# Kernel optimization log

Hardware: AMD Instinct MI355X
Metric: run time of the kernel (lower is better)

The kernel has to match this reference:

```python
import jax, jax.numpy as jnp
import numpy as np

N_NODES = 50000
N_EDGES = 800000
D_IN = 128
D_OUT = 128


def _seg_mean(values, seg_ids, num_segments):
    # values: [E, D] gathered messages; seg_ids: [E] destination ids
    s = jax.ops.segment_sum(values, seg_ids, num_segments=num_segments)
    deg = jax.ops.segment_sum(jnp.ones((values.shape[0],), values.dtype), seg_ids,
                              num_segments=num_segments)
    # DGL mean aggregation yields 0 for zero in-degree nodes
    return jnp.where(deg[:, None] > 0, s / jnp.maximum(deg, 1.0)[:, None], 0.0)


def setup_inputs() -> dict:
    key = jax.random.key(0)
    k1, k2, k3, k4, k5 = jax.random.split(key, 5)
    feat = jax.random.normal(k1, (N_NODES, D_IN), dtype=jnp.float32)
    src = jax.random.randint(k2, (N_EDGES,), 0, N_NODES, dtype=jnp.int32)
    dst = jax.random.randint(k3, (N_EDGES,), 0, N_NODES, dtype=jnp.int32)
    W = jax.random.normal(k4, (D_OUT, 3 * D_IN), dtype=jnp.float32) * (1.0 / np.sqrt(3 * D_IN))
    b = jax.random.normal(k5, (D_OUT,), dtype=jnp.float32) * 0.01
    return {"feat": feat, "src": src, "dst": dst, "W": W, "b": b}


def reference(feat, src, dst, W, b):
    n = feat.shape[0]
    # forward direction: message from src -> dst, mean over in-neighbors
    fwd_neigh = _seg_mean(feat[src], dst, n)          # [N, D]
    # backward direction: graph.reverse() swaps src/dst
    bwd_neigh = _seg_mean(feat[dst], src, n)          # [N, D]
    h = jnp.concatenate((feat, fwd_neigh, bwd_neigh), axis=1)  # [N, 3D]
    return h @ W.T + b
```

## Files before the change

kernel.cpp:

```cpp
#include <hip/hip_runtime.h>

#define DIM 128
#define CAP 64
#define CHUNK 2048

typedef __attribute__((ext_vector_type(8))) short bf16x8;
typedef __attribute__((ext_vector_type(4))) float f32x4;
typedef __attribute__((ext_vector_type(2))) float f32x2;

__device__ __forceinline__ unsigned short f2b(float f) {
  unsigned int u = __float_as_uint(f);
  return (unsigned short)((u + 0x7FFFu + ((u >> 16) & 1u)) >> 16);
}
__device__ __forceinline__ float blo(unsigned int v) { return __uint_as_float(v << 16); }
__device__ __forceinline__ float bhi(unsigned int v) { return __uint_as_float(v & 0xFFFF0000u); }

__global__ __launch_bounds__(256) void k_prepbin(
    const float* __restrict__ feat, const float* __restrict__ W,
    const int* __restrict__ src, const int* __restrict__ dst,
    unsigned short* __restrict__ featb, unsigned short* __restrict__ Wb,
    unsigned int* __restrict__ scrF, unsigned int* __restrict__ scrB,
    int* __restrict__ offsF, int* __restrict__ offsB, int N, int E, int nblk) {
  __shared__ int fc[256], bc[256], fo[256], bo[256], sa[256], sb2[256];
  __shared__ unsigned int linf[CHUNK], linb[CHUNK];
  const int t = threadIdx.x;

  if (blockIdx.x >= nblk) {
    int i = (blockIdx.x - nblk) * 256 + t;
    int ftotal = N * (DIM / 4);
    if (i < ftotal) {
      float4 v = ((const float4*)feat)[i];
      ushort4 o; o.x = f2b(v.x); o.y = f2b(v.y); o.z = f2b(v.z); o.w = f2b(v.w);
      ((ushort4*)featb)[i] = o;
    }
    const int wtotal = DIM * 3 * DIM / 4;
    if (i < wtotal) {
      float4 v = ((const float4*)W)[i];
      ushort4 o; o.x = f2b(v.x); o.y = f2b(v.y); o.z = f2b(v.z); o.w = f2b(v.w);
      ((ushort4*)Wb)[i] = o;
    }
    return;
  }

  const int base = blockIdx.x * CHUNK;
  const int n = min(CHUNK, E - base);
  fc[t] = 0; bc[t] = 0;
  __syncthreads();
  int fbk[8], fsl[8], bsl[8], bbk[8];
  unsigned int fvv[8], bvv[8];
  #pragma unroll
  for (int j = 0; j < 8; ++j) {
    int e = base + j * 256 + t;
    fbk[j] = -1;
    if (e < E) {
      int s = src[e], d = dst[e];
      fbk[j] = d >> 8; fvv[j] = ((unsigned int)(d & 255) << 16) | (unsigned int)s;
      bbk[j] = s >> 8; bvv[j] = ((unsigned int)(s & 255) << 16) | (unsigned int)d;
      fsl[j] = atomicAdd(&fc[fbk[j]], 1);
      bsl[j] = atomicAdd(&bc[bbk[j]], 1);
    }
  }
  __syncthreads();
  sa[t] = fc[t]; sb2[t] = bc[t];
  __syncthreads();
  #pragma unroll
  for (int s = 1; s < 256; s <<= 1) {
    int va = sa[t] + ((t >= s) ? sa[t - s] : 0);
    int vb = sb2[t] + ((t >= s) ? sb2[t - s] : 0);
    __syncthreads();
    sa[t] = va; sb2[t] = vb;
    __syncthreads();
  }
  fo[t] = sa[t] - fc[t];
  bo[t] = sb2[t] - bc[t];
  __syncthreads();
  #pragma unroll
  for (int j = 0; j < 8; ++j) {
    if (fbk[j] >= 0) {
      linf[fo[fbk[j]] + fsl[j]] = fvv[j];
      linb[bo[bbk[j]] + bsl[j]] = bvv[j];
    }
  }
  offsF[blockIdx.x * 256 + t] = fo[t];
  offsB[blockIdx.x * 256 + t] = bo[t];
  __syncthreads();
  for (int k = t; k < n; k += 256) {
    scrF[base + k] = linf[k];
    scrB[base + k] = linb[k];
  }
}

__global__ __launch_bounds__(512) void k_gemmcsr(
    const unsigned short* __restrict__ featb, const unsigned short* __restrict__ Wb,
    const float* __restrict__ bias, unsigned short* __restrict__ g1b,
    unsigned char* __restrict__ g2f8, unsigned char* __restrict__ g3f8,
    const unsigned int* __restrict__ scrF, const unsigned int* __restrict__ scrB,
    const int* __restrict__ offsF, const int* __restrict__ offsB,
    unsigned short* __restrict__ fnbr, unsigned short* __restrict__ bnbr,
    int* __restrict__ degF, int* __restrict__ degB,
    int N, int E, int nblk, int nbkt) {
  __shared__ int ncnt[256];
  __shared__ unsigned short nbuf[256][CAP];
  const int t = threadIdx.x;

  if (blockIdx.x < (unsigned)(2 * nbkt)) {
    const int b = blockIdx.x >> 1;
    const int dir = blockIdx.x & 1;
    const unsigned int* scr = dir ? scrB : scrF;
    const int* offs = dir ? offsB : offsF;
    if (t < 256) ncnt[t] = 0;
    __syncthreads();
    for (int i = t; i < nblk; i += 512) {
      int o = offs[i * 256 + b];
      int n = min(CHUNK, E - i * CHUNK);
      int nxt = (b < 255) ? offs[i * 256 + b + 1] : n;
      int cb = i * CHUNK;
      for (int k = o; k < nxt; ++k) {
        unsigned int v = scr[cb + k];
        int node8 = v >> 16;
        int slot = atomicAdd(&ncnt[node8], 1);
        if (slot < CAP) nbuf[node8][slot] = (unsigned short)(v & 0xFFFFu);
      }
    }
    __syncthreads();
    const int node0 = b * 256;
    const int nvalid = min(256, N - node0);
    if (nvalid <= 0) return;
    unsigned short* outp = (dir ? bnbr : fnbr) + (size_t)node0 * CAP;
    for (int idx = t; idx < nvalid * CAP; idx += 512)
      outp[idx] = nbuf[idx >> 6][idx & 63];
    int* deg = dir ? degB : degF;
    for (int u = t; u < nvalid; u += 512) deg[node0 + u] = ncnt[u];
    return;
  }

  const int gid = blockIdx.x - 2 * nbkt;
  const int wave = t >> 6, lane = t & 63;
  const int lr = lane & 15, lk = lane >> 4;
  const int nc = gid >> 6;
  const int W0 = (gid & 63) * 8 + wave;
  const int TW = 64 * 8;

  bf16x8 bf[4][4];
  #pragma unroll
  for (int kc = 0; kc < 4; ++kc)
    #pragma unroll
    for (int nf = 0; nf < 4; ++nf) {
      int n = nc * 64 + nf * 16 + lr;
      bf[kc][nf] = *(const bf16x8*)(Wb + (size_t)(n & 127) * 384 + (n >> 7) * 128
                                       + kc * 32 + lk * 8);
    }
  float bv[4];
  if (nc < 2) {
    #pragma unroll
    for (int nf = 0; nf < 4; ++nf) bv[nf] = bias[nc * 64 + nf * 16 + lr];
  }

  const int T = N >> 4;
  int tt = W0;
  bf16x8 a[4];
  if (tt < T) {
    #pragma unroll
    for (int kc = 0; kc < 4; ++kc)
      a[kc] = *(const bf16x8*)(featb + (size_t)(tt * 16 + lr) * DIM + kc * 32 + lk * 8);
  }
  while (tt < T) {
    const int tn = tt + TW;
    bf16x8 an[4];
    if (tn < T) {
      #pragma unroll
      for (int kc = 0; kc < 4; ++kc)
        an[kc] = *(const bf16x8*)(featb + (size_t)(tn * 16 + lr) * DIM + kc * 32 + lk * 8);
    }
    const int m0 = tt * 16;
    f32x4 acc[4];
    #pragma unroll
    for (int nf = 0; nf < 4; ++nf) acc[nf] = (f32x4){0.f, 0.f, 0.f, 0.f};
    #pragma unroll
    for (int kc = 0; kc < 4; ++kc)
      #pragma unroll
      for (int nf = 0; nf < 4; ++nf)
        acc[nf] = __builtin_amdgcn_mfma_f32_16x16x32_bf16(a[kc], bf[kc][nf], acc[nf], 0, 0, 0);
    if (nc < 2) {
      #pragma unroll
      for (int nf = 0; nf < 4; ++nf)
        #pragma unroll
        for (int j = 0; j < 4; ++j)
          g1b[(size_t)(m0 + lk * 4 + j) * DIM + nc * 64 + nf * 16 + lr] =
              f2b(acc[nf][j] + bv[nf]);
    } else {
      unsigned char* gp = (nc < 4) ? g2f8 : g3f8;
      const int c0 = (nc & 1) * 64;
      #pragma unroll
      for (int nf = 0; nf < 4; ++nf)
        #pragma unroll
        for (int j = 0; j < 4; ++j) {
          unsigned int p8 = __builtin_amdgcn_cvt_pk_fp8_f32(acc[nf][j], acc[nf][j], 0, 0);
          gp[(size_t)(m0 + lk * 4 + j) * DIM + c0 + nf * 16 + lr] = (unsigned char)p8;
        }
    }
    #pragma unroll
    for (int kc = 0; kc < 4; ++kc) a[kc] = an[kc];
    tt = tn;
  }
}

__global__ void k_aggregate(const unsigned char* __restrict__ g2f8,
                            const unsigned char* __restrict__ g3f8,
                            const unsigned short* __restrict__ g1b,
                            const int* __restrict__ degF, const int* __restrict__ degB,
                            const unsigned short* __restrict__ fnbr,
                            const unsigned short* __restrict__ bnbr,
                            float* __restrict__ out, int N) {
  int node = blockIdx.x * (blockDim.x >> 6) + (threadIdx.x >> 6);
  if (node >= N) return;
  const int lane = threadIdx.x & 63;
  const int qg = lane >> 4;
  const int sub = lane & 15;

  const int degf = degF[node], degb = degB[node];
  const int capf = min(degf, CAP), capb = min(degb, CAP);
  const int fid = fnbr[(size_t)node * CAP + lane];
  const int bid = bnbr[(size_t)node * CAP + lane];

  const uint2* gf = (const uint2*)g2f8;
  const uint2* gb = (const uint2*)g3f8;
  f32x2 f01 = {0.f, 0.f}, f23 = {0.f, 0.f}, f45 = {0.f, 0.f}, f67 = {0.f, 0.f};
  f32x2 b01 = {0.f, 0.f}, b23 = {0.f, 0.f}, b45 = {0.f, 0.f}, b67 = {0.f, 0.f};
  const int gmax = (max(capf, capb) + 3) >> 2;
  #pragma unroll 8
  for (int g = 0; g < gmax; ++g) {
    int k = 4 * g + qg;
    int rf = __shfl(fid, k);
    int rb = __shfl(bid, k);
    if (k < capf) {
      uint2 v = gf[(size_t)rf * 16 + sub];
      f01 += __builtin_amdgcn_cvt_pk_f32_fp8(v.x, 0);
      f23 += __builtin_amdgcn_cvt_pk_f32_fp8(v.x, 1);
      f45 += __builtin_amdgcn_cvt_pk_f32_fp8(v.y, 0);
      f67 += __builtin_amdgcn_cvt_pk_f32_fp8(v.y, 1);
    }
    if (k < capb) {
      uint2 v = gb[(size_t)rb * 16 + sub];
      b01 += __builtin_amdgcn_cvt_pk_f32_fp8(v.x, 0);
      b23 += __builtin_amdgcn_cvt_pk_f32_fp8(v.x, 1);
      b45 += __builtin_amdgcn_cvt_pk_f32_fp8(v.y, 0);
      b67 += __builtin_amdgcn_cvt_pk_f32_fp8(v.y, 1);
    }
  }
  float fa0 = f01[0], fa1 = f01[1], fa2 = f23[0], fa3 = f23[1];
  float fa4 = f45[0], fa5 = f45[1], fa6 = f67[0], fa7 = f67[1];
  float ba0 = b01[0], ba1 = b01[1], ba2 = b23[0], ba3 = b23[1];
  float ba4 = b45[0], ba5 = b45[1], ba6 = b67[0], ba7 = b67[1];
  fa0 += __shfl_xor(fa0, 16); fa0 += __shfl_xor(fa0, 32);
  fa1 += __shfl_xor(fa1, 16); fa1 += __shfl_xor(fa1, 32);
  fa2 += __shfl_xor(fa2, 16); fa2 += __shfl_xor(fa2, 32);
  fa3 += __shfl_xor(fa3, 16); fa3 += __shfl_xor(fa3, 32);
  fa4 += __shfl_xor(fa4, 16); fa4 += __shfl_xor(fa4, 32);
  fa5 += __shfl_xor(fa5, 16); fa5 += __shfl_xor(fa5, 32);
  fa6 += __shfl_xor(fa6, 16); fa6 += __shfl_xor(fa6, 32);
  fa7 += __shfl_xor(fa7, 16); fa7 += __shfl_xor(fa7, 32);
  ba0 += __shfl_xor(ba0, 16); ba0 += __shfl_xor(ba0, 32);
  ba1 += __shfl_xor(ba1, 16); ba1 += __shfl_xor(ba1, 32);
  ba2 += __shfl_xor(ba2, 16); ba2 += __shfl_xor(ba2, 32);
  ba3 += __shfl_xor(ba3, 16); ba3 += __shfl_xor(ba3, 32);
  ba4 += __shfl_xor(ba4, 16); ba4 += __shfl_xor(ba4, 32);
  ba5 += __shfl_xor(ba5, 16); ba5 += __shfl_xor(ba5, 32);
  ba6 += __shfl_xor(ba6, 16); ba6 += __shfl_xor(ba6, 32);
  ba7 += __shfl_xor(ba7, 16); ba7 += __shfl_xor(ba7, 32);

  if (lane < 16) {
    const float sf = (degf > 0) ? 1.0f / (float)degf : 0.0f;
    const float sb = (degb > 0) ? 1.0f / (float)degb : 0.0f;
    uint4 g1v = ((const uint4*)g1b)[(size_t)node * 16 + lane];
    float4 u, v;
    u.x = blo(g1v.x) + fa0 * sf + ba0 * sb;
    u.y = bhi(g1v.x) + fa1 * sf + ba1 * sb;
    u.z = blo(g1v.y) + fa2 * sf + ba2 * sb;
    u.w = bhi(g1v.y) + fa3 * sf + ba3 * sb;
    v.x = blo(g1v.z) + fa4 * sf + ba4 * sb;
    v.y = bhi(g1v.z) + fa5 * sf + ba5 * sb;
    v.z = blo(g1v.w) + fa6 * sf + ba6 * sb;
    v.w = bhi(g1v.w) + fa7 * sf + ba7 * sb;
    float* op = out + (size_t)node * DIM + lane * 8;
    *(float4*)op = u; *(float4*)(op + 4) = v;
  }
}

extern "C" void kernel_launch(void* const* d_in, const int* in_sizes, int n_in,
                              void* d_out, int out_size, void* d_ws, size_t ws_size,
                              hipStream_t stream) {
  (void)n_in; (void)out_size; (void)ws_size;
  const float* feat = (const float*)d_in[0];
  const int*   src  = (const int*)d_in[1];
  const int*   dst  = (const int*)d_in[2];
  const float* W    = (const float*)d_in[3];
  const float* bias = (const float*)d_in[4];
  float* out = (float*)d_out;
  const int N = in_sizes[0] / DIM;
  const int E = in_sizes[1];
  const int nblk = (E + CHUNK - 1) / CHUNK;
  const int nbkt = (N + 255) / 256;

  char* ws = (char*)d_ws;
  size_t off = 0;
  auto take = [&](size_t bytes) -> void* {
    off = (off + 255) & ~(size_t)255;
    void* p = ws + off;
    off += bytes;
    return p;
  };
  unsigned int* scrF = (unsigned int*)take((size_t)nblk * CHUNK * 4);
  unsigned int* scrB = (unsigned int*)take((size_t)nblk * CHUNK * 4);
  int* offsF = (int*)take((size_t)nblk * 256 * 4);
  int* offsB = (int*)take((size_t)nblk * 256 * 4);
  unsigned short* fnbr = (unsigned short*)take((size_t)N * CAP * 2);
  unsigned short* bnbr = (unsigned short*)take((size_t)N * CAP * 2);
  int* degF = (int*)take((size_t)N * 4);
  int* degB = (int*)take((size_t)N * 4);
  unsigned short* featb = (unsigned short*)take((size_t)N * DIM * 2);
  unsigned short* Wb    = (unsigned short*)take((size_t)DIM * 3 * DIM * 2);
  unsigned short* g1b   = (unsigned short*)take((size_t)N * DIM * 2);
  unsigned char*  g2f8  = (unsigned char*)take((size_t)N * DIM);
  unsigned char*  g3f8  = (unsigned char*)take((size_t)N * DIM);

  const int prep_blocks = (N * 32 + 255) / 256;
  k_prepbin<<<nblk + prep_blocks, 256, 0, stream>>>(
      feat, W, src, dst, featb, Wb, scrF, scrB, offsF, offsB, N, E, nblk);
  k_gemmcsr<<<2 * nbkt + 384, 512, 0, stream>>>(
      featb, Wb, bias, g1b, g2f8, g3f8, scrF, scrB, offsF, offsB,
      fnbr, bnbr, degF, degB, N, E, nblk, nbkt);
  k_aggregate<<<(N + 3) / 4, 256, 0, stream>>>(g2f8, g3f8, g1b, degF, degB,
                                               fnbr, bnbr, out, N);
}
```

Before: 101.2 us.

## Fuse bf16 conversion and GEMM into binning kernel, split CSR build out

The projection GEMM now converts feat to bf16 on the fly and holds the whole 384x128 weight matrix in swizzled LDS per block. It runs in the same launch as edge binning, so the separate featb/Wb conversion pass and its global round trip go away. The CSR bucket build moves to its own kernel that starts after binning. CHUNK grows to 4096 and the binning blocks widen to 512 threads. In exchange, each GEMM block uses 96KB of LDS, which caps occupancy, and the CSR build no longer overlaps with the GEMM.

```diff
diff --git a/kernel.cpp b/kernel.cpp
--- a/kernel.cpp
+++ b/kernel.cpp
@@ -2,7 +2,7 @@
 
 #define DIM 128
 #define CAP 64
-#define CHUNK 2048
+#define CHUNK 4096
 
 typedef __attribute__((ext_vector_type(8))) short bf16x8;
 typedef __attribute__((ext_vector_type(4))) float f32x4;
@@ -15,42 +15,100 @@
 __device__ __forceinline__ float blo(unsigned int v) { return __uint_as_float(v << 16); }
 __device__ __forceinline__ float bhi(unsigned int v) { return __uint_as_float(v & 0xFFFF0000u); }
 
-__global__ __launch_bounds__(256) void k_prepbin(
+__global__ __launch_bounds__(512) void k_gemmbin(
     const float* __restrict__ feat, const float* __restrict__ W,
+    const float* __restrict__ bias,
     const int* __restrict__ src, const int* __restrict__ dst,
-    unsigned short* __restrict__ featb, unsigned short* __restrict__ Wb,
+    unsigned short* __restrict__ g1b, unsigned char* __restrict__ g2f8,
+    unsigned char* __restrict__ g3f8,
     unsigned int* __restrict__ scrF, unsigned int* __restrict__ scrB,
-    int* __restrict__ offsF, int* __restrict__ offsB, int N, int E, int nblk) {
-  __shared__ int fc[256], bc[256], fo[256], bo[256], sa[256], sb2[256];
-  __shared__ unsigned int linf[CHUNK], linb[CHUNK];
+    int* __restrict__ offsF, int* __restrict__ offsB,
+    int N, int E, int G, int nblk) {
+  __shared__ __align__(16) unsigned char smem[98304];
   const int t = threadIdx.x;
 
-  if (blockIdx.x >= nblk) {
-    int i = (blockIdx.x - nblk) * 256 + t;
-    int ftotal = N * (DIM / 4);
-    if (i < ftotal) {
-      float4 v = ((const float4*)feat)[i];
-      ushort4 o; o.x = f2b(v.x); o.y = f2b(v.y); o.z = f2b(v.z); o.w = f2b(v.w);
-      ((ushort4*)featb)[i] = o;
-    }
-    const int wtotal = DIM * 3 * DIM / 4;
-    if (i < wtotal) {
-      float4 v = ((const float4*)W)[i];
-      ushort4 o; o.x = f2b(v.x); o.y = f2b(v.y); o.z = f2b(v.z); o.w = f2b(v.w);
-      ((ushort4*)Wb)[i] = o;
+  if ((int)blockIdx.x < G) {
+    for (int i = t; i < 12288; i += 512) {
+      int flat = i * 4;
+      int o = flat / 384;
+      int kk = flat - o * 384;
+      int n = (kk >> 7) * 128 + o;
+      int k0 = kk & 127;
+      float4 v = *(const float4*)(W + flat);
+      ushort4 u; u.x = f2b(v.x); u.y = f2b(v.y); u.z = f2b(v.z); u.w = f2b(v.w);
+      *(ushort4*)(smem + ((n * 256 + k0 * 2) ^ ((n & 7) << 4))) = u;
+    }
+    __syncthreads();
+
+    const int wave = t >> 6, lane = t & 63;
+    const int lr = lane & 15, lk = lane >> 4;
+    float bv[8];
+    #pragma unroll
+    for (int i = 0; i < 8; ++i) bv[i] = bias[i * 16 + lr];
+
+    const int T = N >> 4;
+    const int TW = G * 8;
+    for (int tile = blockIdx.x * 8 + wave; tile < T; tile += TW) {
+      const int m0 = tile * 16;
+      bf16x8 a[4];
+      #pragma unroll
+      for (int kc = 0; kc < 4; ++kc) {
+        const float* p = feat + (size_t)(m0 + lr) * DIM + kc * 32 + lk * 8;
+        float4 u = *(const float4*)p;
+        float4 w = *(const float4*)(p + 4);
+        bf16x8 r;
+        r[0] = f2b(u.x); r[1] = f2b(u.y); r[2] = f2b(u.z); r[3] = f2b(u.w);
+        r[4] = f2b(w.x); r[5] = f2b(w.y); r[6] = f2b(w.z); r[7] = f2b(w.w);
+        a[kc] = r;
+      }
+      #pragma unroll
+      for (int nf = 0; nf < 24; ++nf) {
+        f32x4 acc = (f32x4){0.f, 0.f, 0.f, 0.f};
+        const int n = nf * 16 + lr;
+        #pragma unroll
+        for (int kc = 0; kc < 4; ++kc) {
+          bf16x8 bw = *(const bf16x8*)(smem +
+              ((n * 256 + kc * 64 + lk * 16) ^ ((n & 7) << 4)));
+          acc = __builtin_amdgcn_mfma_f32_16x16x32_bf16(a[kc], bw, acc, 0, 0, 0);
+        }
+        const int sec = nf >> 3;
+        const int c0 = (nf & 7) * 16 + lr;
+        if (sec == 0) {
+          #pragma unroll
+          for (int j = 0; j < 4; ++j)
+            g1b[(size_t)(m0 + lk * 4 + j) * DIM + c0] = f2b(acc[j] + bv[nf & 7]);
+        } else {
+          unsigned char* gp = (sec == 1) ? g2f8 : g3f8;
+          #pragma unroll
+          for (int j = 0; j < 4; ++j) {
+            unsigned int p8 = __builtin_amdgcn_cvt_pk_fp8_f32(acc[j], acc[j], 0, 0);
+            gp[(size_t)(m0 + lk * 4 + j) * DIM + c0] = (unsigned char)p8;
+          }
+        }
+      }
     }
     return;
   }
 
-  const int base = blockIdx.x * CHUNK;
+  int* fc = (int*)smem;
+  int* bc = fc + 256;
+  int* fo = bc + 256;
+  int* bo = fo + 256;
+  int* sa = bo + 256;
+  int* sb2 = sa + 256;
+  unsigned int* linf = (unsigned int*)(sb2 + 256);
+  unsigned int* linb = linf + CHUNK;
+
+  const int bid = blockIdx.x - G;
+  const int base = bid * CHUNK;
   const int n = min(CHUNK, E - base);
-  fc[t] = 0; bc[t] = 0;
+  if (t < 256) { fc[t] = 0; bc[t] = 0; }
   __syncthreads();
   int fbk[8], fsl[8], bsl[8], bbk[8];
   unsigned int fvv[8], bvv[8];
   #pragma unroll
   for (int j = 0; j < 8; ++j) {
-    int e = base + j * 256 + t;
+    int e = base + j * 512 + t;
     fbk[j] = -1;
     if (e < E) {
       int s = src[e], d = dst[e];
@@ -61,18 +119,19 @@
     }
   }
   __syncthreads();
-  sa[t] = fc[t]; sb2[t] = bc[t];
-  __syncthreads();
-  #pragma unroll
+  if (t < 256) { sa[t] = fc[t]; sb2[t] = bc[t]; }
+  __syncthreads();
   for (int s = 1; s < 256; s <<= 1) {
-    int va = sa[t] + ((t >= s) ? sa[t - s] : 0);
-    int vb = sb2[t] + ((t >= s) ? sb2[t - s] : 0);
+    int va = 0, vb = 0;
+    if (t < 256) {
+      va = sa[t] + ((t >= s) ? sa[t - s] : 0);
+      vb = sb2[t] + ((t >= s) ? sb2[t - s] : 0);
+    }
     __syncthreads();
-    sa[t] = va; sb2[t] = vb;
+    if (t < 256) { sa[t] = va; sb2[t] = vb; }
     __syncthreads();
   }
-  fo[t] = sa[t] - fc[t];
-  bo[t] = sb2[t] - bc[t];
+  if (t < 256) { fo[t] = sa[t] - fc[t]; bo[t] = sb2[t] - bc[t]; }
   __syncthreads();
   #pragma unroll
   for (int j = 0; j < 8; ++j) {
@@ -81,128 +140,55 @@
       linb[bo[bbk[j]] + bsl[j]] = bvv[j];
     }
   }
-  offsF[blockIdx.x * 256 + t] = fo[t];
-  offsB[blockIdx.x * 256 + t] = bo[t];
-  __syncthreads();
-  for (int k = t; k < n; k += 256) {
+  if (t < 256) {
+    offsF[bid * 256 + t] = fo[t];
+    offsB[bid * 256 + t] = bo[t];
+  }
+  __syncthreads();
+  for (int k = t; k < n; k += 512) {
     scrF[base + k] = linf[k];
     scrB[base + k] = linb[k];
   }
 }
 
-__global__ __launch_bounds__(512) void k_gemmcsr(
-    const unsigned short* __restrict__ featb, const unsigned short* __restrict__ Wb,
-    const float* __restrict__ bias, unsigned short* __restrict__ g1b,
-    unsigned char* __restrict__ g2f8, unsigned char* __restrict__ g3f8,
-    const unsigned int* __restrict__ scrF, const unsigned int* __restrict__ scrB,
-    const int* __restrict__ offsF, const int* __restrict__ offsB,
-    unsigned short* __restrict__ fnbr, unsigned short* __restrict__ bnbr,
-    int* __restrict__ degF, int* __restrict__ degB,
-    int N, int E, int nblk, int nbkt) {
+__global__ __launch_bounds__(512) void k_csr(const unsigned int* __restrict__ scrF,
+                                             const unsigned int* __restrict__ scrB,
+                                             const int* __restrict__ offsF,
+                                             const int* __restrict__ offsB,
+                                             unsigned short* __restrict__ fnbr,
+                                             unsigned short* __restrict__ bnbr,
+                                             int* __restrict__ degF, int* __restrict__ degB,
+                                             int N, int E, int nblk) {
   __shared__ int ncnt[256];
   __shared__ unsigned short nbuf[256][CAP];
+  const int b = blockIdx.x;
+  const int dir = blockIdx.y;
+  const unsigned int* scr = dir ? scrB : scrF;
+  const int* offs = dir ? offsB : offsF;
   const int t = threadIdx.x;
-
-  if (blockIdx.x < (unsigned)(2 * nbkt)) {
-    const int b = blockIdx.x >> 1;
-    const int dir = blockIdx.x & 1;
-    const unsigned int* scr = dir ? scrB : scrF;
-    const int* offs = dir ? offsB : offsF;
-    if (t < 256) ncnt[t] = 0;
-    __syncthreads();
-    for (int i = t; i < nblk; i += 512) {
-      int o = offs[i * 256 + b];
-      int n = min(CHUNK, E - i * CHUNK);
-      int nxt = (b < 255) ? offs[i * 256 + b + 1] : n;
-      int cb = i * CHUNK;
-      for (int k = o; k < nxt; ++k) {
-        unsigned int v = scr[cb + k];
-        int node8 = v >> 16;
-        int slot = atomicAdd(&ncnt[node8], 1);
-        if (slot < CAP) nbuf[node8][slot] = (unsigned short)(v & 0xFFFFu);
-      }
-    }
-    __syncthreads();
-    const int node0 = b * 256;
-    const int nvalid = min(256, N - node0);
-    if (nvalid <= 0) return;
-    unsigned short* outp = (dir ? bnbr : fnbr) + (size_t)node0 * CAP;
-    for (int idx = t; idx < nvalid * CAP; idx += 512)
-      outp[idx] = nbuf[idx >> 6][idx & 63];
-    int* deg = dir ? degB : degF;
-    for (int u = t; u < nvalid; u += 512) deg[node0 + u] = ncnt[u];
-    return;
-  }
-
-  const int gid = blockIdx.x - 2 * nbkt;
-  const int wave = t >> 6, lane = t & 63;
-  const int lr = lane & 15, lk = lane >> 4;
-  const int nc = gid >> 6;
-  const int W0 = (gid & 63) * 8 + wave;
-  const int TW = 64 * 8;
-
-  bf16x8 bf[4][4];
-  #pragma unroll
-  for (int kc = 0; kc < 4; ++kc)
-    #pragma unroll
-    for (int nf = 0; nf < 4; ++nf) {
-      int n = nc * 64 + nf * 16 + lr;
-      bf[kc][nf] = *(const bf16x8*)(Wb + (size_t)(n & 127) * 384 + (n >> 7) * 128
-                                       + kc * 32 + lk * 8);
-    }
-  float bv[4];
-  if (nc < 2) {
-    #pragma unroll
-    for (int nf = 0; nf < 4; ++nf) bv[nf] = bias[nc * 64 + nf * 16 + lr];
-  }
-
-  const int T = N >> 4;
-  int tt = W0;
-  bf16x8 a[4];
-  if (tt < T) {
-    #pragma unroll
-    for (int kc = 0; kc < 4; ++kc)
-      a[kc] = *(const bf16x8*)(featb + (size_t)(tt * 16 + lr) * DIM + kc * 32 + lk * 8);
-  }
-  while (tt < T) {
-    const int tn = tt + TW;
-    bf16x8 an[4];
-    if (tn < T) {
-      #pragma unroll
-      for (int kc = 0; kc < 4; ++kc)
-        an[kc] = *(const bf16x8*)(featb + (size_t)(tn * 16 + lr) * DIM + kc * 32 + lk * 8);
-    }
-    const int m0 = tt * 16;
-    f32x4 acc[4];
-    #pragma unroll
-    for (int nf = 0; nf < 4; ++nf) acc[nf] = (f32x4){0.f, 0.f, 0.f, 0.f};
-    #pragma unroll
-    for (int kc = 0; kc < 4; ++kc)
-      #pragma unroll
-      for (int nf = 0; nf < 4; ++nf)
-        acc[nf] = __builtin_amdgcn_mfma_f32_16x16x32_bf16(a[kc], bf[kc][nf], acc[nf], 0, 0, 0);
-    if (nc < 2) {
-      #pragma unroll
-      for (int nf = 0; nf < 4; ++nf)
-        #pragma unroll
-        for (int j = 0; j < 4; ++j)
-          g1b[(size_t)(m0 + lk * 4 + j) * DIM + nc * 64 + nf * 16 + lr] =
-              f2b(acc[nf][j] + bv[nf]);
-    } else {
-      unsigned char* gp = (nc < 4) ? g2f8 : g3f8;
-      const int c0 = (nc & 1) * 64;
-      #pragma unroll
-      for (int nf = 0; nf < 4; ++nf)
-        #pragma unroll
-        for (int j = 0; j < 4; ++j) {
-          unsigned int p8 = __builtin_amdgcn_cvt_pk_fp8_f32(acc[nf][j], acc[nf][j], 0, 0);
-          gp[(size_t)(m0 + lk * 4 + j) * DIM + c0 + nf * 16 + lr] = (unsigned char)p8;
-        }
-    }
-    #pragma unroll
-    for (int kc = 0; kc < 4; ++kc) a[kc] = an[kc];
-    tt = tn;
-  }
+  if (t < 256) ncnt[t] = 0;
+  __syncthreads();
+  for (int i = t; i < nblk; i += 512) {
+    int o = offs[i * 256 + b];
+    int n = min(CHUNK, E - i * CHUNK);
+    int nxt = (b < 255) ? offs[i * 256 + b + 1] : n;
+    int cb = i * CHUNK;
+    for (int k = o; k < nxt; ++k) {
+      unsigned int v = scr[cb + k];
+      int node8 = v >> 16;
+      int slot = atomicAdd(&ncnt[node8], 1);
+      if (slot < CAP) nbuf[node8][slot] = (unsigned short)(v & 0xFFFFu);
+    }
+  }
+  __syncthreads();
+  const int node0 = b * 256;
+  const int nvalid = min(256, N - node0);
+  if (nvalid <= 0) return;
+  unsigned short* outp = (dir ? bnbr : fnbr) + (size_t)node0 * CAP;
+  for (int idx = t; idx < nvalid * CAP; idx += 512)
+    outp[idx] = nbuf[idx >> 6][idx & 63];
+  int* deg = dir ? degB : degF;
+  for (int u = t; u < nvalid; u += 512) deg[node0 + u] = ncnt[u];
 }
 
 __global__ void k_aggregate(const unsigned char* __restrict__ g2f8,
@@ -301,6 +287,7 @@
   const int E = in_sizes[1];
   const int nblk = (E + CHUNK - 1) / CHUNK;
   const int nbkt = (N + 255) / 256;
+  const int G = 192;
 
   char* ws = (char*)d_ws;
   size_t off = 0;
@@ -318,18 +305,15 @@
   unsigned short* bnbr = (unsigned short*)take((size_t)N * CAP * 2);
   int* degF = (int*)take((size_t)N * 4);
   int* degB = (int*)take((size_t)N * 4);
-  unsigned short* featb = (unsigned short*)take((size_t)N * DIM * 2);
-  unsigned short* Wb    = (unsigned short*)take((size_t)DIM * 3 * DIM * 2);
-  unsigned short* g1b   = (unsigned short*)take((size_t)N * DIM * 2);
-  unsigned char*  g2f8  = (unsigned char*)take((size_t)N * DIM);
-  unsigned char*  g3f8  = (unsigned char*)take((size_t)N * DIM);
-
-  const int prep_blocks = (N * 32 + 255) / 256;
-  k_prepbin<<<nblk + prep_blocks, 256, 0, stream>>>(
-      feat, W, src, dst, featb, Wb, scrF, scrB, offsF, offsB, N, E, nblk);
-  k_gemmcsr<<<2 * nbkt + 384, 512, 0, stream>>>(
-      featb, Wb, bias, g1b, g2f8, g3f8, scrF, scrB, offsF, offsB,
-      fnbr, bnbr, degF, degB, N, E, nblk, nbkt);
+  unsigned short* g1b  = (unsigned short*)take((size_t)N * DIM * 2);
+  unsigned char*  g2f8 = (unsigned char*)take((size_t)N * DIM);
+  unsigned char*  g3f8 = (unsigned char*)take((size_t)N * DIM);
+
+  k_gemmbin<<<G + nblk, 512, 0, stream>>>(
+      feat, W, bias, src, dst, g1b, g2f8, g3f8,
+      scrF, scrB, offsF, offsB, N, E, G, nblk);
+  k_csr<<<dim3(nbkt, 2), 512, 0, stream>>>(scrF, scrB, offsF, offsB,
+                                           fnbr, bnbr, degF, degB, N, E, nblk);
   k_aggregate<<<(N + 3) / 4, 256, 0, stream>>>(g2f8, g3f8, g1b, degF, degB,
                                                fnbr, bnbr, out, N);
 }
```

Measured after the change: 96.30 us. -4.9%, faster.
